# Kernel tuning notes

Hardware: AMD Instinct MI355X
Metric: run time of the kernel (lower is better)

## Reference

```python
import jax, jax.numpy as jnp
import numpy as np

R = 3.9
EPS = 0.3
BETA = 0.15
STEPS = 15


def setup_inputs() -> dict:
    key = jax.random.key(0)
    k1, k2 = jax.random.split(key)
    drive = jax.random.uniform(k1, (2048, 1, 16384), dtype=jnp.float32)
    K = jnp.abs(jax.random.uniform(k2, (3,), dtype=jnp.float32))
    K = K / K.sum()
    return {"drive": drive, "K": K}


def reference(drive, K):
    # Circular 3-tap conv: torch conv1d is cross-correlation, padded circularly,
    # so local[i] = K[0]*m[i-1] + K[1]*m[i] + K[2]*m[i+1] (indices mod L).
    def step(grid, _):
        mapped = R * grid * (1.0 - grid)
        local = (K[0] * jnp.roll(mapped, 1, axis=-1)
                 + K[1] * mapped
                 + K[2] * jnp.roll(mapped, -1, axis=-1))
        physics = (1.0 - EPS) * mapped + EPS * local
        grid = (1.0 - BETA) * physics + BETA * drive
        return grid, None

    grid, _ = jax.lax.scan(step, drive, None, length=STEPS)
    return jnp.clip(grid, 0.0001, 1.0 - 0.0001)
```

## Files before the change

kernel.cpp:

```cpp
#include <hip/hip_runtime.h>


constexpr float Rc    = 3.9f;
constexpr float EPSc  = 0.3f;
constexpr float BETAc = 0.15f;
constexpr int   STEPS = 15;
constexpr int   L     = 16384;
constexpr int   CE    = 17;
constexpr int   SEG   = 1024;
constexpr int   GHOST = 32;
constexpr int   EXT   = SEG + 2*GHOST;
constexpr int   TPB   = 256;
constexpr int   WPB   = TPB / 64;

__global__ __launch_bounds__(TPB)
void cml1d_kernel(const float* __restrict__ drive,
                  const float* __restrict__ K,
                  float* __restrict__ out) {
    __shared__ float lds[WPB][EXT];

    const int lane = threadIdx.x & 63;
    const int wv   = threadIdx.x >> 6;
    const int gw   = blockIdx.x * WPB + wv;
    const int row  = gw >> 4;
    const int seg  = gw & 15;
    const size_t rowbase = (size_t)row * L;
    const int wbase = seg * SEG - GHOST;

    #pragma unroll
    for (int j = 0; j < 5; ++j) {
        int f = j * 64 + lane;
        if (f < EXT / 4) {
            int e   = wbase + f * 4;
            int idx = e & (L - 1);
            float4 v = *reinterpret_cast<const float4*>(drive + rowbase + idx);
            *reinterpret_cast<float4*>(&lds[wv][f * 4]) = v;
        }
    }
    __builtin_amdgcn_wave_barrier();

    const float K0 = K[0], K1 = K[1], K2 = K[2];
    const float A  = (1.0f - BETAc) * (1.0f - EPSc);
    const float B  = (1.0f - BETAc) * EPSc;
    const float d0 = Rc * (B * K0);
    const float d1 = Rc * (A + B * K1);
    const float d2 = Rc * (B * K2);

    float g[CE], bd[CE];
    #pragma unroll
    for (int i = 0; i < CE; ++i) {
        float v = lds[wv][lane * CE + i];
        g[i]  = v;
        bd[i] = BETAc * v;
    }

    const int addrL = ((lane - 1) & 63) << 2;
    const int addrR = ((lane + 1) & 63) << 2;

    for (int s = 0; s < STEPS; ++s) {
        float mh0  = fmaf(-g[0],      g[0],      g[0]);
        float mhT  = fmaf(-g[CE - 1], g[CE - 1], g[CE - 1]);
        float mleft  = __int_as_float(
            __builtin_amdgcn_ds_bpermute(addrL, __float_as_int(mhT)));
        float mright = __int_as_float(
            __builtin_amdgcn_ds_bpermute(addrR, __float_as_int(mh0)));

        float mprev = mh0;
        float mcur  = fmaf(-g[1], g[1], g[1]);
        const float m1s = mcur;
        float mTs = mcur;
        #pragma unroll
        for (int i = 1; i < CE - 1; ++i) {
            float mnext;
            if (i == CE - 2) { mnext = mhT; mTs = mcur; }
            else {
                float gv = g[i + 1];
                mnext = fmaf(-gv, gv, gv);
            }
            g[i] = fmaf(d0, mprev, fmaf(d1, mcur, fmaf(d2, mnext, bd[i])));
            mprev = mcur;
            mcur  = mnext;
        }
        g[0]      = fmaf(d0, mleft, fmaf(d1, mh0, fmaf(d2, m1s,    bd[0])));
        g[CE - 1] = fmaf(d0, mTs,   fmaf(d1, mhT, fmaf(d2, mright, bd[CE - 1])));
    }

    __builtin_amdgcn_wave_barrier();
    #pragma unroll
    for (int i = 0; i < CE; ++i) lds[wv][lane * CE + i] = g[i];
    __builtin_amdgcn_wave_barrier();

    const float lo = 0.0001f;
    const float hi = 0.9999f;
    #pragma unroll
    for (int j = 0; j < 4; ++j) {
        int f = j * 64 + lane;
        float4 v = *reinterpret_cast<float4*>(&lds[wv][GHOST + f * 4]);
        v.x = fminf(fmaxf(v.x, lo), hi);
        v.y = fminf(fmaxf(v.y, lo), hi);
        v.z = fminf(fmaxf(v.z, lo), hi);
        v.w = fminf(fmaxf(v.w, lo), hi);
        *reinterpret_cast<float4*>(out + rowbase + seg * SEG + f * 4) = v;
    }
}

extern "C" void kernel_launch(void* const* d_in, const int* in_sizes, int n_in,
                              void* d_out, int out_size, void* d_ws, size_t ws_size,
                              hipStream_t stream) {
    const float* drive = (const float*)d_in[0];
    const float* K     = (const float*)d_in[1];
    float* out         = (float*)d_out;
    const int rows   = in_sizes[0] / L;
    const int gwaves = rows * (L / SEG);
    const int blocks = gwaves / WPB;
    cml1d_kernel<<<dim3(blocks), dim3(TPB), 0, stream>>>(drive, K, out);
}
```

Before: 232.8 us.

## Make waves persistent over four segments and prefetch the next segment's input

The launch now uses a fixed grid of 2048 blocks, and each wave loops over four row segments instead of handling one. While it computes the current segment, the wave loads the next segment's drive data into registers, so global load latency overlaps with the 15-step stencil. The clamp now uses fmed3 in place of separate min and max. The grid size is hardcoded, which ties correctness to the 2048-row input size, and the prefetch buffer adds register pressure.

```diff
diff --git a/kernel.cpp b/kernel.cpp
--- a/kernel.cpp
+++ b/kernel.cpp
@@ -12,6 +12,8 @@
 constexpr int   EXT   = SEG + 2*GHOST;
 constexpr int   TPB   = 256;
 constexpr int   WPB   = TPB / 64;
+constexpr int   T     = 4;
+constexpr int   NBLK  = 2048;
 
 __global__ __launch_bounds__(TPB)
 void cml1d_kernel(const float* __restrict__ drive,
@@ -21,23 +23,7 @@
 
     const int lane = threadIdx.x & 63;
     const int wv   = threadIdx.x >> 6;
-    const int gw   = blockIdx.x * WPB + wv;
-    const int row  = gw >> 4;
-    const int seg  = gw & 15;
-    const size_t rowbase = (size_t)row * L;
-    const int wbase = seg * SEG - GHOST;
-
-    #pragma unroll
-    for (int j = 0; j < 5; ++j) {
-        int f = j * 64 + lane;
-        if (f < EXT / 4) {
-            int e   = wbase + f * 4;
-            int idx = e & (L - 1);
-            float4 v = *reinterpret_cast<const float4*>(drive + rowbase + idx);
-            *reinterpret_cast<float4*>(&lds[wv][f * 4]) = v;
-        }
-    }
-    __builtin_amdgcn_wave_barrier();
+    const int gw0  = blockIdx.x * WPB + wv;
 
     const float K0 = K[0], K1 = K[1], K2 = K[2];
     const float A  = (1.0f - BETAc) * (1.0f - EPSc);
@@ -46,61 +32,109 @@
     const float d1 = Rc * (A + B * K1);
     const float d2 = Rc * (B * K2);
 
-    float g[CE], bd[CE];
-    #pragma unroll
-    for (int i = 0; i < CE; ++i) {
-        float v = lds[wv][lane * CE + i];
-        g[i]  = v;
-        bd[i] = BETAc * v;
-    }
-
     const int addrL = ((lane - 1) & 63) << 2;
     const int addrR = ((lane + 1) & 63) << 2;
 
-    for (int s = 0; s < STEPS; ++s) {
-        float mh0  = fmaf(-g[0],      g[0],      g[0]);
-        float mhT  = fmaf(-g[CE - 1], g[CE - 1], g[CE - 1]);
-        float mleft  = __int_as_float(
-            __builtin_amdgcn_ds_bpermute(addrL, __float_as_int(mhT)));
-        float mright = __int_as_float(
-            __builtin_amdgcn_ds_bpermute(addrR, __float_as_int(mh0)));
-
-        float mprev = mh0;
-        float mcur  = fmaf(-g[1], g[1], g[1]);
-        const float m1s = mcur;
-        float mTs = mcur;
+    float4 p[5];
+    {
+        const int gw  = gw0;
+        const int row = gw >> 4, seg = gw & 15;
+        const size_t rb = (size_t)row * L;
+        const int wbase = seg * SEG - GHOST;
         #pragma unroll
-        for (int i = 1; i < CE - 1; ++i) {
-            float mnext;
-            if (i == CE - 2) { mnext = mhT; mTs = mcur; }
-            else {
-                float gv = g[i + 1];
-                mnext = fmaf(-gv, gv, gv);
+        for (int j = 0; j < 5; ++j) {
+            int f = j * 64 + lane;
+            if (f < EXT / 4) {
+                int idx = (wbase + f * 4) & (L - 1);
+                p[j] = *reinterpret_cast<const float4*>(drive + rb + idx);
             }
-            g[i] = fmaf(d0, mprev, fmaf(d1, mcur, fmaf(d2, mnext, bd[i])));
-            mprev = mcur;
-            mcur  = mnext;
         }
-        g[0]      = fmaf(d0, mleft, fmaf(d1, mh0, fmaf(d2, m1s,    bd[0])));
-        g[CE - 1] = fmaf(d0, mTs,   fmaf(d1, mhT, fmaf(d2, mright, bd[CE - 1])));
     }
 
-    __builtin_amdgcn_wave_barrier();
-    #pragma unroll
-    for (int i = 0; i < CE; ++i) lds[wv][lane * CE + i] = g[i];
-    __builtin_amdgcn_wave_barrier();
+    #pragma unroll 1
+    for (int t = 0; t < T; ++t) {
+        const int gw  = t * (NBLK * WPB) + gw0;
+        const int row = gw >> 4, seg = gw & 15;
+        const size_t rb = (size_t)row * L;
 
-    const float lo = 0.0001f;
-    const float hi = 0.9999f;
-    #pragma unroll
-    for (int j = 0; j < 4; ++j) {
-        int f = j * 64 + lane;
-        float4 v = *reinterpret_cast<float4*>(&lds[wv][GHOST + f * 4]);
-        v.x = fminf(fmaxf(v.x, lo), hi);
-        v.y = fminf(fmaxf(v.y, lo), hi);
-        v.z = fminf(fmaxf(v.z, lo), hi);
-        v.w = fminf(fmaxf(v.w, lo), hi);
-        *reinterpret_cast<float4*>(out + rowbase + seg * SEG + f * 4) = v;
+        #pragma unroll
+        for (int j = 0; j < 5; ++j) {
+            int f = j * 64 + lane;
+            if (f < EXT / 4)
+                *reinterpret_cast<float4*>(&lds[wv][f * 4]) = p[j];
+        }
+        __builtin_amdgcn_wave_barrier();
+
+        float g[CE], bd[CE];
+        #pragma unroll
+        for (int i = 0; i < CE; ++i) {
+            float v = lds[wv][lane * CE + i];
+            g[i]  = v;
+            bd[i] = BETAc * v;
+        }
+
+        if (t < T - 1) {
+            const int gw2  = (t + 1) * (NBLK * WPB) + gw0;
+            const int row2 = gw2 >> 4, seg2 = gw2 & 15;
+            const size_t rb2 = (size_t)row2 * L;
+            const int wb2 = seg2 * SEG - GHOST;
+            #pragma unroll
+            for (int j = 0; j < 5; ++j) {
+                int f = j * 64 + lane;
+                if (f < EXT / 4) {
+                    int idx = (wb2 + f * 4) & (L - 1);
+                    p[j] = *reinterpret_cast<const float4*>(drive + rb2 + idx);
+                }
+            }
+        }
+        __builtin_amdgcn_sched_barrier(0);
+
+        for (int s = 0; s < STEPS; ++s) {
+            float mh0  = fmaf(-g[0],      g[0],      g[0]);
+            float mhT  = fmaf(-g[CE - 1], g[CE - 1], g[CE - 1]);
+            float mleft  = __int_as_float(
+                __builtin_amdgcn_ds_bpermute(addrL, __float_as_int(mhT)));
+            float mright = __int_as_float(
+                __builtin_amdgcn_ds_bpermute(addrR, __float_as_int(mh0)));
+
+            float mprev = mh0;
+            float mcur  = fmaf(-g[1], g[1], g[1]);
+            const float m1s = mcur;
+            float mTs = mcur;
+            #pragma unroll
+            for (int i = 1; i < CE - 1; ++i) {
+                float mnext;
+                if (i == CE - 2) { mnext = mhT; mTs = mcur; }
+                else {
+                    float gv = g[i + 1];
+                    mnext = fmaf(-gv, gv, gv);
+                }
+                g[i] = fmaf(d0, mprev, fmaf(d1, mcur, fmaf(d2, mnext, bd[i])));
+                mprev = mcur;
+                mcur  = mnext;
+            }
+            g[0]      = fmaf(d0, mleft, fmaf(d1, mh0, fmaf(d2, m1s,    bd[0])));
+            g[CE - 1] = fmaf(d0, mTs,   fmaf(d1, mhT, fmaf(d2, mright, bd[CE - 1])));
+        }
+
+        __builtin_amdgcn_wave_barrier();
+        #pragma unroll
+        for (int i = 0; i < CE; ++i) lds[wv][lane * CE + i] = g[i];
+        __builtin_amdgcn_wave_barrier();
+
+        const float lo = 0.0001f;
+        const float hi = 0.9999f;
+        #pragma unroll
+        for (int j = 0; j < 4; ++j) {
+            int f = j * 64 + lane;
+            float4 v = *reinterpret_cast<float4*>(&lds[wv][GHOST + f * 4]);
+            v.x = __builtin_amdgcn_fmed3f(v.x, lo, hi);
+            v.y = __builtin_amdgcn_fmed3f(v.y, lo, hi);
+            v.z = __builtin_amdgcn_fmed3f(v.z, lo, hi);
+            v.w = __builtin_amdgcn_fmed3f(v.w, lo, hi);
+            *reinterpret_cast<float4*>(out + rb + seg * SEG + f * 4) = v;
+        }
+        __builtin_amdgcn_wave_barrier();
     }
 }
 
@@ -110,8 +144,5 @@
     const float* drive = (const float*)d_in[0];
     const float* K     = (const float*)d_in[1];
     float* out         = (float*)d_out;
-    const int rows   = in_sizes[0] / L;
-    const int gwaves = rows * (L / SEG);
-    const int blocks = gwaves / WPB;
-    cml1d_kernel<<<dim3(blocks), dim3(TPB), 0, stream>>>(drive, K, out);
+    cml1d_kernel<<<dim3(NBLK), dim3(TPB), 0, stream>>>(drive, K, out);
 }
```

Measured after the change: 264.6 us. 1.14x slower.

## Make kernel persistent with double-buffered async global-to-LDS prefetch of next segment

Applied to the files above, without the earlier changes.

Launches a fixed grid of 1024 blocks, each looping over T segments per wave. While one segment is computed, the next segment's input is loaded straight into a second LDS buffer with global_load_lds, hiding load latency behind the 15-step compute. The clamp now uses fmed3 instead of min/max. The cost is doubled LDS per block and hand-tuned vmcnt waits, which are fragile if the compiler issues other memory operations. The grid size and T also assume the segment count divides evenly by 4096.

```diff
diff --git a/kernel.cpp b/kernel.cpp
--- a/kernel.cpp
+++ b/kernel.cpp
@@ -1,4 +1,5 @@
 #include <hip/hip_runtime.h>
+#include <stdint.h>
 
 
 constexpr float Rc    = 3.9f;
@@ -12,32 +13,21 @@
 constexpr int   EXT   = SEG + 2*GHOST;
 constexpr int   TPB   = 256;
 constexpr int   WPB   = TPB / 64;
+constexpr int   NBLK  = 1024;
+
+typedef const __attribute__((address_space(1))) float gfloat;
+typedef __attribute__((address_space(3))) float lfloat;
 
 __global__ __launch_bounds__(TPB)
 void cml1d_kernel(const float* __restrict__ drive,
                   const float* __restrict__ K,
-                  float* __restrict__ out) {
-    __shared__ float lds[WPB][EXT];
+                  float* __restrict__ out,
+                  int T) {
+    __shared__ float lds[WPB][2][EXT];
 
     const int lane = threadIdx.x & 63;
     const int wv   = threadIdx.x >> 6;
-    const int gw   = blockIdx.x * WPB + wv;
-    const int row  = gw >> 4;
-    const int seg  = gw & 15;
-    const size_t rowbase = (size_t)row * L;
-    const int wbase = seg * SEG - GHOST;
-
-    #pragma unroll
-    for (int j = 0; j < 5; ++j) {
-        int f = j * 64 + lane;
-        if (f < EXT / 4) {
-            int e   = wbase + f * 4;
-            int idx = e & (L - 1);
-            float4 v = *reinterpret_cast<const float4*>(drive + rowbase + idx);
-            *reinterpret_cast<float4*>(&lds[wv][f * 4]) = v;
-        }
-    }
-    __builtin_amdgcn_wave_barrier();
+    const int gw0  = blockIdx.x * WPB + wv;
 
     const float K0 = K[0], K1 = K[1], K2 = K[2];
     const float A  = (1.0f - BETAc) * (1.0f - EPSc);
@@ -46,61 +36,100 @@
     const float d1 = Rc * (A + B * K1);
     const float d2 = Rc * (B * K2);
 
-    float g[CE], bd[CE];
-    #pragma unroll
-    for (int i = 0; i < CE; ++i) {
-        float v = lds[wv][lane * CE + i];
-        g[i]  = v;
-        bd[i] = BETAc * v;
-    }
-
     const int addrL = ((lane - 1) & 63) << 2;
     const int addrR = ((lane + 1) & 63) << 2;
 
-    for (int s = 0; s < STEPS; ++s) {
-        float mh0  = fmaf(-g[0],      g[0],      g[0]);
-        float mhT  = fmaf(-g[CE - 1], g[CE - 1], g[CE - 1]);
-        float mleft  = __int_as_float(
-            __builtin_amdgcn_ds_bpermute(addrL, __float_as_int(mhT)));
-        float mright = __int_as_float(
-            __builtin_amdgcn_ds_bpermute(addrR, __float_as_int(mh0)));
+    float g[CE], bd[CE];
 
-        float mprev = mh0;
-        float mcur  = fmaf(-g[1], g[1], g[1]);
-        const float m1s = mcur;
-        float mTs = mcur;
+    auto prefetch = [&](int gw, float* buf) {
+        const int row = gw >> 4, seg = gw & 15;
+        const float* base = drive + (size_t)row * L;
+        const int wb = seg * SEG - GHOST;
         #pragma unroll
-        for (int i = 1; i < CE - 1; ++i) {
-            float mnext;
-            if (i == CE - 2) { mnext = mhT; mTs = mcur; }
-            else {
-                float gv = g[i + 1];
-                mnext = fmaf(-gv, gv, gv);
+        for (int j = 0; j < 4; ++j) {
+            int idx = (wb + j * 256 + lane * 4) & (L - 1);
+            __builtin_amdgcn_global_load_lds((gfloat*)(base + idx),
+                                             (lfloat*)(buf + j * 256), 16, 0, 0);
+        }
+        int idx = (wb + 1024 + lane) & (L - 1);
+        __builtin_amdgcn_global_load_lds((gfloat*)(base + idx),
+                                         (lfloat*)(buf + 1024), 4, 0, 0);
+    };
+    auto unpack = [&](const float* buf) {
+        #pragma unroll
+        for (int i = 0; i < CE; ++i) {
+            float v = buf[lane * CE + i];
+            g[i]  = v;
+            bd[i] = BETAc * v;
+        }
+    };
+
+    prefetch(gw0, &lds[wv][0][0]);
+    asm volatile("s_waitcnt vmcnt(0)" ::: "memory");
+    unpack(&lds[wv][0][0]);
+
+    int cur = 0;
+    #pragma unroll 1
+    for (int t = 0; t < T; ++t) {
+        if (t < T - 1)
+            prefetch((t + 1) * (NBLK * WPB) + gw0, &lds[wv][cur ^ 1][0]);
+        __builtin_amdgcn_sched_barrier(0);
+
+        for (int s = 0; s < STEPS; ++s) {
+            float mh0  = fmaf(-g[0],      g[0],      g[0]);
+            float mhT  = fmaf(-g[CE - 1], g[CE - 1], g[CE - 1]);
+            float mleft  = __int_as_float(
+                __builtin_amdgcn_ds_bpermute(addrL, __float_as_int(mhT)));
+            float mright = __int_as_float(
+                __builtin_amdgcn_ds_bpermute(addrR, __float_as_int(mh0)));
+
+            float mprev = mh0;
+            float mcur  = fmaf(-g[1], g[1], g[1]);
+            const float m1s = mcur;
+            float mTs = mcur;
+            #pragma unroll
+            for (int i = 1; i < CE - 1; ++i) {
+                float mnext;
+                if (i == CE - 2) { mnext = mhT; mTs = mcur; }
+                else {
+                    float gv = g[i + 1];
+                    mnext = fmaf(-gv, gv, gv);
+                }
+                g[i] = fmaf(d0, mprev, fmaf(d1, mcur, fmaf(d2, mnext, bd[i])));
+                mprev = mcur;
+                mcur  = mnext;
             }
-            g[i] = fmaf(d0, mprev, fmaf(d1, mcur, fmaf(d2, mnext, bd[i])));
-            mprev = mcur;
-            mcur  = mnext;
+            g[0]      = fmaf(d0, mleft, fmaf(d1, mh0, fmaf(d2, m1s,    bd[0])));
+            g[CE - 1] = fmaf(d0, mTs,   fmaf(d1, mhT, fmaf(d2, mright, bd[CE - 1])));
         }
-        g[0]      = fmaf(d0, mleft, fmaf(d1, mh0, fmaf(d2, m1s,    bd[0])));
-        g[CE - 1] = fmaf(d0, mTs,   fmaf(d1, mhT, fmaf(d2, mright, bd[CE - 1])));
-    }
 
-    __builtin_amdgcn_wave_barrier();
-    #pragma unroll
-    for (int i = 0; i < CE; ++i) lds[wv][lane * CE + i] = g[i];
-    __builtin_amdgcn_wave_barrier();
+        const int gw  = t * (NBLK * WPB) + gw0;
+        const int row = gw >> 4, seg = gw & 15;
+        float* tb = &lds[wv][cur][0];
+        __builtin_amdgcn_wave_barrier();
+        #pragma unroll
+        for (int i = 0; i < CE; ++i) tb[lane * CE + i] = g[i];
+        __builtin_amdgcn_wave_barrier();
 
-    const float lo = 0.0001f;
-    const float hi = 0.9999f;
-    #pragma unroll
-    for (int j = 0; j < 4; ++j) {
-        int f = j * 64 + lane;
-        float4 v = *reinterpret_cast<float4*>(&lds[wv][GHOST + f * 4]);
-        v.x = fminf(fmaxf(v.x, lo), hi);
-        v.y = fminf(fmaxf(v.y, lo), hi);
-        v.z = fminf(fmaxf(v.z, lo), hi);
-        v.w = fminf(fmaxf(v.w, lo), hi);
-        *reinterpret_cast<float4*>(out + rowbase + seg * SEG + f * 4) = v;
+        const float lo = 0.0001f;
+        const float hi = 0.9999f;
+        float* op = out + (size_t)row * L + seg * SEG;
+        #pragma unroll
+        for (int j = 0; j < 4; ++j) {
+            int f = j * 64 + lane;
+            float4 v = *reinterpret_cast<float4*>(&tb[GHOST + f * 4]);
+            v.x = __builtin_amdgcn_fmed3f(v.x, lo, hi);
+            v.y = __builtin_amdgcn_fmed3f(v.y, lo, hi);
+            v.z = __builtin_amdgcn_fmed3f(v.z, lo, hi);
+            v.w = __builtin_amdgcn_fmed3f(v.w, lo, hi);
+            *reinterpret_cast<float4*>(op + f * 4) = v;
+        }
+
+        if (t < T - 1) {
+            asm volatile("s_waitcnt vmcnt(4)" ::: "memory");
+            unpack(&lds[wv][cur ^ 1][0]);
+            cur ^= 1;
+        }
     }
 }
 
@@ -112,6 +141,6 @@
     float* out         = (float*)d_out;
     const int rows   = in_sizes[0] / L;
     const int gwaves = rows * (L / SEG);
-    const int blocks = gwaves / WPB;
-    cml1d_kernel<<<dim3(blocks), dim3(TPB), 0, stream>>>(drive, K, out);
+    const int T      = gwaves / (NBLK * WPB);
+    cml1d_kernel<<<dim3(NBLK), dim3(TPB), 0, stream>>>(drive, K, out, T);
 }
```

Result: no change. 236.9 us (+1.8%).
